# Optimization experiments

Measured on AMD Instinct MI355X. Metric: run time of the kernel, lower is better.

The kernel has to match this reference:

```python
import jax, jax.numpy as jnp
import numpy as np

# Structural hyperparams (mirror init_kwargs)
G, Q, C, D = 2, 8, 1024, 8          # groups, quantizers/group, codebook_size, codebook_dim
DIMS = 1024                          # residual_fsq.dim
DPG = DIMS // G                      # dim per group (project_out output)
B, L = 4, 4096                       # batch, frame length
UP_K, UP_S = 4, 2                    # upsample ConvTranspose1d kernel/stride
HEAD_K, HEAD_OUT = 7, 512            # head Conv1d kernel / out channels


def setup_inputs() -> dict:
    key = jax.random.key(0)
    ks = jax.random.split(key, 8)
    indices = jax.random.randint(ks[0], (B, G * Q, L), 0, C, dtype=jnp.int64)
    codebooks = jax.random.normal(ks[1], (G, Q, C, D), jnp.float32)
    scales = jax.random.uniform(ks[2], (G, Q, D), jnp.float32, 0.5, 2.0)
    W_out = jax.random.normal(ks[3], (G, D, DPG), jnp.float32) * (1.0 / np.sqrt(D))
    b_out = jnp.zeros((G, DPG), jnp.float32)
    W_up = jax.random.normal(ks[4], (DIMS, DIMS, UP_K), jnp.float32) * 0.02   # IOH layout
    b_up = jnp.zeros((DIMS,), jnp.float32)
    W_head = jax.random.normal(ks[5], (HEAD_OUT, DIMS, HEAD_K), jnp.float32) * 0.02  # OIH
    b_head = jnp.zeros((HEAD_OUT,), jnp.float32)
    return dict(indices=indices, codebooks=codebooks, scales=scales,
                W_out=W_out, b_out=b_out, W_up=W_up, b_up=b_up,
                W_head=W_head, b_head=b_head)


def reference(indices, codebooks, scales, W_out, b_out, W_up, b_up, W_head, b_head):
    b, gq, l = indices.shape
    g, q = codebooks.shape[0], codebooks.shape[1]
    # [B, G*Q, L] -> [G, B, L, Q]  (matches view + permute in forward)
    idx = indices.reshape(b, g, q, l).transpose(1, 0, 3, 2)
    mask = idx == -1                              # dropout-padded codes
    idx0 = jnp.where(mask, 0, idx)
    # gather codes per (group, quantizer): codebooks[g, q, idx0[g,b,l,q]] -> [G,B,L,Q,D]
    g_ix = jnp.arange(g)[:, None, None, None]
    q_ix = jnp.arange(q)[None, None, None, :]
    codes = codebooks[g_ix, q_ix, idx0]
    # mask, scale, sum over quantizers (residual sum)
    codes = jnp.where(mask[..., None], 0.0, codes) * scales[:, None, None, :, :]
    summed = codes.sum(axis=3)                    # [G,B,L,D]
    # per-group project_out: Linear(D -> DPG)
    z = jnp.einsum('gbld,gde->gble', summed, W_out) + b_out[:, None, None, :]
    # concat groups along feature dim -> [B, L, DIMS], then NCH for convs
    z_q = z.transpose(1, 2, 0, 3).reshape(b, l, g * z.shape[-1])
    zc = z_q.transpose(0, 2, 1)                   # [B, DIMS, L]
    # upsample: ConvTranspose1d(DIMS->DIMS, k=4, stride=2) -> [B, DIMS, 2L]
    zu = jax.lax.conv_transpose(zc, W_up, strides=(UP_S,), padding='SAME',
                                dimension_numbers=('NCH', 'IOH', 'NCH'))
    zu = zu + b_up[None, :, None]
    # head: Conv1d(DIMS -> HEAD_OUT, k=7, same padding)
    x = jax.lax.conv_general_dilated(zu, W_head, window_strides=(1,), padding='SAME',
                                     dimension_numbers=('NCH', 'OIH', 'NCH'))
    x = x + b_head[None, :, None]
    return x
```

## Files before the change

### kernel.cpp

```cpp
#include <hip/hip_runtime.h>
#include <hip/hip_bf16.h>

typedef __attribute__((ext_vector_type(8))) short bf16x8;
typedef __attribute__((ext_vector_type(4))) float f32x4;

#define GQ 16
#define L_IN 4096
#define T_UP 8192
#define CB 1024
#define ZROWS 4098
#define UROWS 8198

__device__ __forceinline__ void gload16(const void* g, void* l) {
    __builtin_amdgcn_global_load_lds((const __attribute__((address_space(1))) void*)g,
                                     (__attribute__((address_space(3))) void*)l, 16, 0, 0);
}

#define SBR() do { asm volatile("" ::: "memory");                 \
                   __builtin_amdgcn_sched_barrier(0);             \
                   __builtin_amdgcn_s_barrier();                  \
                   __builtin_amdgcn_sched_barrier(0);             \
                   asm volatile("" ::: "memory"); } while (0)
#define LGKM() do { asm volatile("s_waitcnt lgkmcnt(0)" ::: "memory"); \
                    __builtin_amdgcn_sched_barrier(0); } while (0)
#define VMW(n) do { __builtin_amdgcn_sched_barrier(0); \
                    asm volatile("s_waitcnt vmcnt(" #n ")" ::: "memory"); \
                    __builtin_amdgcn_sched_barrier(0); } while (0)

#define MM(MH, NH) do {                                                          \
    __builtin_amdgcn_s_setprio(1);                                               \
    _Pragma("unroll") for (int j_ = 0; j_ < 4; ++j_)                             \
      _Pragma("unroll") for (int n_ = 0; n_ < 2; ++n_)                           \
        _Pragma("unroll") for (int s_ = 0; s_ < 2; ++s_)                         \
          acc[(MH)*4 + j_][(NH)*2 + n_] = __builtin_amdgcn_mfma_f32_16x16x32_bf16( \
              af[j_][s_], bq[(NH)*2 + n_][s_], acc[(MH)*4 + j_][(NH)*2 + n_],    \
              0, 0, 0);                                                          \
    __builtin_amdgcn_s_setprio(0);                                               \
} while (0)

__global__ __launch_bounds__(256) void zero_pads(__hip_bfloat16* __restrict__ zp,
                                                 __hip_bfloat16* __restrict__ zup) {
    int idx = blockIdx.x * 256 + threadIdx.x;
    if (idx < 8192) {
        int b = idx >> 11, rs = (idx >> 10) & 1, c = idx & 1023;
        size_t row = (size_t)b * ZROWS + (rs ? (ZROWS - 1) : 0);
        zp[row * 1024 + c] = __float2bfloat16(0.f);
    } else if (idx < 8192 + 24576) {
        int rem = idx - 8192;
        int b = rem / 6144, r2 = rem % 6144;
        int r6 = r2 >> 10, c = r2 & 1023;
        size_t row = (size_t)b * UROWS + (r6 < 3 ? r6 : (UROWS - 6 + r6));
        zup[row * 1024 + c] = __float2bfloat16(0.f);
    }
}

__global__ __launch_bounds__(256) void repack_up(const float* __restrict__ Wup,
                                                 __hip_bfloat16* __restrict__ Wr) {
    int idx = blockIdx.x * 256 + threadIdx.x;
    int kk = idx >> 20;
    int co = (idx >> 10) & 1023;
    int ci = idx & 1023;
    Wr[idx] = __float2bfloat16(Wup[((ci << 10) + co) * 4 + kk]);
}

__global__ __launch_bounds__(256) void repack_head(const float* __restrict__ Wh,
                                                   __hip_bfloat16* __restrict__ Wr) {
    int idx = blockIdx.x * 256 + threadIdx.x;
    int kk = idx >> 19;
    int rem = idx & ((1 << 19) - 1);
    int o = rem >> 10;
    int ci = rem & 1023;
    Wr[idx] = __float2bfloat16(Wh[(o * 1024 + ci) * 7 + kk]);
}

__global__ __launch_bounds__(256) void dequant_project(
    const int* __restrict__ indices, const float* __restrict__ codebooks,
    const float* __restrict__ scales, const float* __restrict__ Wout,
    const float* __restrict__ bout, __hip_bfloat16* __restrict__ z)
{
    __shared__ float w_lds[8192];
    __shared__ float b_lds[1024];
    __shared__ float part[128];
    __shared__ float summed[16];
    int tid = threadIdx.x;
    for (int k = tid; k < 8192; k += 256) w_lds[k] = Wout[k];
    for (int k = tid; k < 1024; k += 256) b_lds[k] = bout[k];
    int p0 = blockIdx.x * 16;
    int b  = p0 >> 12;
    int l0 = p0 & 4095;
    __syncthreads();
    for (int i = 0; i < 16; ++i) {
        int l = l0 + i;
        if (tid < 128) {
            int gq = tid >> 3;
            int d  = tid & 7;
            int idx = indices[(b * GQ + gq) * L_IN + l];
            float v = 0.f;
            if (idx >= 0) {
                int ic = (idx < CB) ? idx : 0;
                v = codebooks[(gq * CB + ic) * 8 + d] * scales[gq * 8 + d];
            }
            part[tid] = v;
        }
        __syncthreads();
        if (tid < 16) {
            int g = tid >> 3, d = tid & 7;
            float s = 0.f;
            for (int q = 0; q < 8; ++q) s += part[(g * 8 + q) * 8 + d];
            summed[tid] = s;
        }
        __syncthreads();
        #pragma unroll
        for (int j = 0; j < 4; ++j) {
            int c = tid + j * 256;
            int g = c >> 9;
            float acc = b_lds[c];
            #pragma unroll
            for (int d = 0; d < 8; ++d)
                acc += summed[g * 8 + d] * w_lds[(g * 8 + d) * 512 + (c & 511)];
            z[((size_t)b * ZROWS + l + 1) * 1024 + c] = __float2bfloat16(acc);
        }
        __syncthreads();
    }
}


__global__ __launch_bounds__(512, 2) void conv_up_mfma(
    const __hip_bfloat16* __restrict__ zp, const __hip_bfloat16* __restrict__ Wr,
    const float* __restrict__ bup, __hip_bfloat16* __restrict__ zup)
{
    __shared__ __hip_bfloat16 Als[2][256][64];
    __shared__ __hip_bfloat16 Bls[2][256][64];
    const int tid = threadIdx.x;
    const int lane = tid & 63;
    const int w = tid >> 6;
    const int wm = w >> 2, wn = w & 3;
    const int l15 = lane & 15, kq = lane >> 4;
    const int m0  = blockIdx.x * 256;
    const int co0 = blockIdx.y * 256;
    const int b = blockIdx.z >> 1, P = blockIdx.z & 1;
    const int NT = 32, NIT = 16;

    const __hip_bfloat16* abase = zp + ((size_t)b * ZROWS + m0 + P) * 1024;
    const __hip_bfloat16* bbase = Wr + ((size_t)P * 1024 + co0) * 1024;

    auto stage = [&](int kt, int part) {
        if (kt >= NT) return;
        const int buf = kt & 1;
        const int j = kt >> 4, ci0 = (kt & 15) << 6;
        const int rb = (part & 1) << 7;
        const __hip_bfloat16* src;
        __hip_bfloat16* dst;
        if (part < 2) { src = abase + ((size_t)j + rb) * 1024 + ci0;
                        dst = &Als[buf][rb][0]; }
        else          { src = bbase + ((size_t)j * 2048 + rb) * 1024 + ci0;
                        dst = &Bls[buf][rb][0]; }
        #pragma unroll
        for (int it = 0; it < 2; ++it) {
            int chunk = it * 512 + tid;
            int row = chunk >> 3, cs = chunk & 7;
            int cq = cs ^ (row & 7);
            gload16(src + (size_t)row * 1024 + cq * 8,
                    (char*)dst + ((it * 512 + (w << 6)) << 4));
        }
    };

    f32x4 acc[8][4];
    const f32x4 z4 = {0.f, 0.f, 0.f, 0.f};
    #pragma unroll
    for (int i = 0; i < 8; ++i)
        #pragma unroll
        for (int j = 0; j < 4; ++j) acc[i][j] = z4;

    bf16x8 af[4][2], bq[4][2];

    auto rdA = [&](int buf, int mh) {
        #pragma unroll
        for (int j = 0; j < 4; ++j)
            #pragma unroll
            for (int sl = 0; sl < 2; ++sl) {
                int row = (wm << 7) + (mh << 6) + j * 16 + l15;
                int ch = (sl * 4 + kq) ^ (row & 7);
                af[j][sl] = *(const bf16x8*)&Als[buf][row][ch * 8];
            }
    };
    auto rdBlo = [&](int buf) {
        #pragma unroll
        for (int nf = 0; nf < 2; ++nf)
            #pragma unroll
            for (int sl = 0; sl < 2; ++sl) {
                int row = (wn << 6) + nf * 16 + l15;
                int ch = (sl * 4 + kq) ^ (row & 7);
                bq[nf][sl] = *(const bf16x8*)&Bls[buf][row][ch * 8];
            }
    };
    auto rdBhi = [&](int buf) {
        #pragma unroll
        for (int nf = 2; nf < 4; ++nf)
            #pragma unroll
            for (int sl = 0; sl < 2; ++sl) {
                int row = (wn << 6) + nf * 16 + l15;
                int ch = (sl * 4 + kq) ^ (row & 7);
                bq[nf][sl] = *(const bf16x8*)&Bls[buf][row][ch * 8];
            }
    };

    stage(0, 2); stage(0, 3); stage(0, 0); stage(0, 1);
    stage(1, 2); stage(1, 3); stage(1, 0);
    VMW(6);
    SBR();
    rdA(0, 0); rdBlo(0);

    for (int it = 0; it < NIT; ++it) {
        const bool lastit = (it == NIT - 1);
        stage(2 * it + 1, 1);
        SBR(); LGKM();
        MM(0, 0);
        rdBhi(0);
        SBR();
        stage(2 * it + 2, 2);
        SBR(); LGKM();
        MM(0, 1);
        rdA(0, 1);
        SBR();
        stage(2 * it + 2, 3);
        SBR(); LGKM();
        MM(1, 1);
        SBR();
        stage(2 * it + 2, 0);
        if (lastit) { VMW(0); } else { VMW(6); }
        SBR();
        MM(1, 0);
        rdA(1, 0); rdBlo(1);
        SBR();
        stage(2 * it + 2, 1);
        SBR(); LGKM();
        MM(0, 0);
        rdBhi(1);
        SBR();
        stage(2 * it + 3, 2);
        SBR(); LGKM();
        MM(0, 1);
        rdA(1, 1);
        SBR();
        stage(2 * it + 3, 3);
        SBR(); LGKM();
        MM(1, 1);
        SBR();
        stage(2 * it + 3, 0);
        if (!lastit) { VMW(6); }
        SBR();
        MM(1, 0);
        if (!lastit) { rdA(0, 0); rdBlo(0); }
        SBR();
    }

    float bias[4];
    #pragma unroll
    for (int nf = 0; nf < 4; ++nf) bias[nf] = bup[co0 + (wn << 6) + nf * 16 + l15];
    const int mbase = m0 + (wm << 7) + (kq << 2);
    const int cob = co0 + (wn << 6) + l15;
    #pragma unroll
    for (int mf = 0; mf < 8; ++mf)
        #pragma unroll
        for (int e = 0; e < 4; ++e) {
            int m = mbase + mf * 16 + e;
            size_t rowoff = ((size_t)b * UROWS + 3 + P + 2 * m) * 1024;
            #pragma unroll
            for (int nf = 0; nf < 4; ++nf)
                zup[rowoff + cob + nf * 16] = __float2bfloat16(acc[mf][nf][e] + bias[nf]);
        }
}

__global__ __launch_bounds__(512, 2) void conv_head_mfma(
    const __hip_bfloat16* __restrict__ zup, const __hip_bfloat16* __restrict__ Wr,
    const float* __restrict__ bh, float* __restrict__ out)
{
    __shared__ __hip_bfloat16 Als[2][256][64];
    __shared__ __hip_bfloat16 Bls[2][256][64];
    const int tid = threadIdx.x;
    const int lane = tid & 63;
    const int w = tid >> 6;
    const int wm = w >> 2, wn = w & 3;
    const int l15 = lane & 15, kq = lane >> 4;
    const int t0 = blockIdx.x * 256;
    const int o0 = blockIdx.y * 256;
    const int b  = blockIdx.z;
    const int NT = 112, NIT = 56;

    const __hip_bfloat16* bbase = zup + ((size_t)b * UROWS + t0) * 1024;

    auto stage = [&](int kt, int part) {
        if (kt >= NT) return;
        const int buf = kt & 1;
        const int kk = kt >> 4, ci0 = (kt & 15) << 6;
        const int rb = (part & 1) << 7;
        const __hip_bfloat16* src;
        __hip_bfloat16* dst;
        if (part < 2) { src = Wr + ((size_t)(kk * 512 + o0 + rb)) * 1024 + ci0;
                        dst = &Als[buf][rb][0]; }
        else          { src = bbase + ((size_t)(kk + rb)) * 1024 + ci0;
                        dst = &Bls[buf][rb][0]; }
        #pragma unroll
        for (int it = 0; it < 2; ++it) {
            int chunk = it * 512 + tid;
            int row = chunk >> 3, cs = chunk & 7;
            int cq = cs ^ (row & 7);
            gload16(src + (size_t)row * 1024 + cq * 8,
                    (char*)dst + ((it * 512 + (w << 6)) << 4));
        }
    };

    f32x4 acc[8][4];
    const f32x4 z4 = {0.f, 0.f, 0.f, 0.f};
    #pragma unroll
    for (int i = 0; i < 8; ++i)
        #pragma unroll
        for (int j = 0; j < 4; ++j) acc[i][j] = z4;

    bf16x8 af[4][2], bq[4][2];

    auto rdA = [&](int buf, int mh) {
        #pragma unroll
        for (int j = 0; j < 4; ++j)
            #pragma unroll
            for (int sl = 0; sl < 2; ++sl) {
                int row = (wm << 7) + (mh << 6) + j * 16 + l15;
                int ch = (sl * 4 + kq) ^ (row & 7);
                af[j][sl] = *(const bf16x8*)&Als[buf][row][ch * 8];
            }
    };
    auto rdBlo = [&](int buf) {
        #pragma unroll
        for (int nf = 0; nf < 2; ++nf)
            #pragma unroll
            for (int sl = 0; sl < 2; ++sl) {
                int row = (wn << 6) + nf * 16 + l15;
                int ch = (sl * 4 + kq) ^ (row & 7);
                bq[nf][sl] = *(const bf16x8*)&Bls[buf][row][ch * 8];
            }
    };
    auto rdBhi = [&](int buf) {
        #pragma unroll
        for (int nf = 2; nf < 4; ++nf)
            #pragma unroll
            for (int sl = 0; sl < 2; ++sl) {
                int row = (wn << 6) + nf * 16 + l15;
                int ch = (sl * 4 + kq) ^ (row & 7);
                bq[nf][sl] = *(const bf16x8*)&Bls[buf][row][ch * 8];
            }
    };

    stage(0, 2); stage(0, 3); stage(0, 0); stage(0, 1);
    stage(1, 2); stage(1, 3); stage(1, 0);
    VMW(6);
    SBR();
    rdA(0, 0); rdBlo(0);

    for (int it = 0; it < NIT; ++it) {
        const bool lastit = (it == NIT - 1);
        stage(2 * it + 1, 1);
        SBR(); LGKM();
        MM(0, 0);
        rdBhi(0);
        SBR();
        stage(2 * it + 2, 2);
        SBR(); LGKM();
        MM(0, 1);
        rdA(0, 1);
        SBR();
        stage(2 * it + 2, 3);
        SBR(); LGKM();
        MM(1, 1);
        SBR();
        stage(2 * it + 2, 0);
        if (lastit) { VMW(0); } else { VMW(6); }
        SBR();
        MM(1, 0);
        rdA(1, 0); rdBlo(1);
        SBR();
        stage(2 * it + 2, 1);
        SBR(); LGKM();
        MM(0, 0);
        rdBhi(1);
        SBR();
        stage(2 * it + 3, 2);
        SBR(); LGKM();
        MM(0, 1);
        rdA(1, 1);
        SBR();
        stage(2 * it + 3, 3);
        SBR(); LGKM();
        MM(1, 1);
        SBR();
        stage(2 * it + 3, 0);
        if (!lastit) { VMW(6); }
        SBR();
        MM(1, 0);
        if (!lastit) { rdA(0, 0); rdBlo(0); }
        SBR();
    }

    const int obase = o0 + (wm << 7) + (kq << 2);
    const int tbase = t0 + (wn << 6) + l15;
    #pragma unroll
    for (int mf = 0; mf < 8; ++mf)
        #pragma unroll
        for (int e = 0; e < 4; ++e) {
            int o = obase + mf * 16 + e;
            float bias = bh[o];
            size_t rowoff = ((size_t)b * 512 + o) * T_UP + tbase;
            #pragma unroll
            for (int nf = 0; nf < 4; ++nf)
                out[rowoff + nf * 16] = acc[mf][nf][e] + bias;
        }
}

extern "C" void kernel_launch(void* const* d_in, const int* in_sizes, int n_in,
                              void* d_out, int out_size, void* d_ws, size_t ws_size,
                              hipStream_t stream) {
    const int*   indices   = (const int*)d_in[0];
    const float* codebooks = (const float*)d_in[1];
    const float* scales    = (const float*)d_in[2];
    const float* Wout      = (const float*)d_in[3];
    const float* bout      = (const float*)d_in[4];
    const float* Wup       = (const float*)d_in[5];
    const float* bup       = (const float*)d_in[6];
    const float* Wh        = (const float*)d_in[7];
    const float* bh        = (const float*)d_in[8];
    float* out = (float*)d_out;

    __hip_bfloat16* zp    = (__hip_bfloat16*)d_ws;
    __hip_bfloat16* zup   = zp + (size_t)4 * ZROWS * 1024;
    __hip_bfloat16* wr_up = zup + (size_t)4 * UROWS * 1024;
    __hip_bfloat16* wr_h  = wr_up + (size_t)4 * 1024 * 1024;

    zero_pads  <<<dim3(128),   dim3(256), 0, stream>>>(zp, zup);
    repack_up  <<<dim3(16384), dim3(256), 0, stream>>>(Wup, wr_up);
    repack_head<<<dim3(14336), dim3(256), 0, stream>>>(Wh, wr_h);
    dequant_project<<<dim3(1024), dim3(256), 0, stream>>>(indices, codebooks, scales,
                                                          Wout, bout, zp);
    conv_up_mfma  <<<dim3(16, 4, 8), dim3(512), 0, stream>>>(zp, wr_up, bup, zup);
    conv_head_mfma<<<dim3(32, 2, 4), dim3(512), 0, stream>>>(zup, wr_h, bh, out);
}
```

Before: 466.7 us.

## Fold upsample and head convolutions into a single combined-weight GEMM

```diff
diff --git a/kernel.cpp b/kernel.cpp
--- a/kernel.cpp
+++ b/kernel.cpp
@@ -6,10 +6,8 @@
 
 #define GQ 16
 #define L_IN 4096
-#define T_UP 8192
 #define CB 1024
-#define ZROWS 4098
-#define UROWS 8198
+#define ZR 4100
 
 __device__ __forceinline__ void gload16(const void* g, void* l) {
     __builtin_amdgcn_global_load_lds((const __attribute__((address_space(1))) void*)g,
@@ -38,29 +36,17 @@
     __builtin_amdgcn_s_setprio(0);                                               \
 } while (0)
 
-__global__ __launch_bounds__(256) void zero_pads(__hip_bfloat16* __restrict__ zp,
-                                                 __hip_bfloat16* __restrict__ zup) {
+__device__ const int TERM_KK[28]  = {0,1, 0,1,2,3, 2,3,4,5, 4,5,6, 6,
+                                     0, 0,1,2, 1,2,3,4, 3,4,5,6, 5,6};
+__device__ const int TERM_TAP[28] = {1,0, 3,2,1,0, 3,2,1,0, 3,2,1, 3,
+                                     0, 2,1,0, 3,2,1,0, 3,2,1,0, 3,2};
+__device__ const int SLICE_OFF[11] = {0,2,6,10,13,14,15,18,22,26,28};
+
+__global__ __launch_bounds__(256) void zero_pads_z(__hip_bfloat16* __restrict__ zp) {
     int idx = blockIdx.x * 256 + threadIdx.x;
-    if (idx < 8192) {
-        int b = idx >> 11, rs = (idx >> 10) & 1, c = idx & 1023;
-        size_t row = (size_t)b * ZROWS + (rs ? (ZROWS - 1) : 0);
-        zp[row * 1024 + c] = __float2bfloat16(0.f);
-    } else if (idx < 8192 + 24576) {
-        int rem = idx - 8192;
-        int b = rem / 6144, r2 = rem % 6144;
-        int r6 = r2 >> 10, c = r2 & 1023;
-        size_t row = (size_t)b * UROWS + (r6 < 3 ? r6 : (UROWS - 6 + r6));
-        zup[row * 1024 + c] = __float2bfloat16(0.f);
-    }
-}
-
-__global__ __launch_bounds__(256) void repack_up(const float* __restrict__ Wup,
-                                                 __hip_bfloat16* __restrict__ Wr) {
-    int idx = blockIdx.x * 256 + threadIdx.x;
-    int kk = idx >> 20;
-    int co = (idx >> 10) & 1023;
-    int ci = idx & 1023;
-    Wr[idx] = __float2bfloat16(Wup[((ci << 10) + co) * 4 + kk]);
+    int b = idx >> 12, r4 = (idx >> 10) & 3, c = idx & 1023;
+    size_t row = (size_t)b * ZR + (r4 < 2 ? r4 : (ZR - 4 + r4));
+    zp[row * 1024 + c] = __float2bfloat16(0.f);
 }
 
 __global__ __launch_bounds__(256) void repack_head(const float* __restrict__ Wh,
@@ -69,8 +55,18 @@
     int kk = idx >> 19;
     int rem = idx & ((1 << 19) - 1);
     int o = rem >> 10;
-    int ci = rem & 1023;
-    Wr[idx] = __float2bfloat16(Wh[(o * 1024 + ci) * 7 + kk]);
+    int cu = rem & 1023;
+    Wr[idx] = __float2bfloat16(Wh[(o * 1024 + cu) * 7 + kk]);
+}
+
+__global__ __launch_bounds__(256) void repack_upT(const float* __restrict__ Wup,
+                                                  __hip_bfloat16* __restrict__ Wupt) {
+    int idx = blockIdx.x * 256 + threadIdx.x;
+    const float4 w = *(const float4*)&Wup[(size_t)idx * 4];
+    Wupt[idx]           = __float2bfloat16(w.x);
+    Wupt[1048576 + idx] = __float2bfloat16(w.y);
+    Wupt[2097152 + idx] = __float2bfloat16(w.z);
+    Wupt[3145728 + idx] = __float2bfloat16(w.w);
 }
 
 __global__ __launch_bounds__(256) void dequant_project(
@@ -118,16 +114,31 @@
             #pragma unroll
             for (int d = 0; d < 8; ++d)
                 acc += summed[g * 8 + d] * w_lds[(g * 8 + d) * 512 + (c & 511)];
-            z[((size_t)b * ZROWS + l + 1) * 1024 + c] = __float2bfloat16(acc);
+            z[((size_t)b * ZR + l + 2) * 1024 + c] = __float2bfloat16(acc);
         }
         __syncthreads();
     }
 }
 
-
-__global__ __launch_bounds__(512, 2) void conv_up_mfma(
-    const __hip_bfloat16* __restrict__ zp, const __hip_bfloat16* __restrict__ Wr,
-    const float* __restrict__ bup, __hip_bfloat16* __restrict__ zup)
+__global__ __launch_bounds__(64) void bias_combine(const float* __restrict__ Wh,
+                                                   const float* __restrict__ bup,
+                                                   const float* __restrict__ bh,
+                                                   float* __restrict__ bt) {
+    int o = blockIdx.x * 64 + threadIdx.x;
+    float acc = bh[o];
+    const float* wrow = Wh + (size_t)o * 7168;
+    for (int cu = 0; cu < 1024; ++cu) {
+        float ws = 0.f;
+        #pragma unroll
+        for (int kk = 0; kk < 7; ++kk) ws += wrow[cu * 7 + kk];
+        acc += ws * bup[cu];
+    }
+    bt[o] = acc;
+}
+
+__global__ __launch_bounds__(512, 2) void combine_gemm(
+    const __hip_bfloat16* __restrict__ Whr, const __hip_bfloat16* __restrict__ Wupt,
+    float* __restrict__ P32)
 {
     __shared__ __hip_bfloat16 Als[2][256][64];
     __shared__ __hip_bfloat16 Bls[2][256][64];
@@ -136,25 +147,24 @@
     const int w = tid >> 6;
     const int wm = w >> 2, wn = w & 3;
     const int l15 = lane & 15, kq = lane >> 4;
-    const int m0  = blockIdx.x * 256;
-    const int co0 = blockIdx.y * 256;
-    const int b = blockIdx.z >> 1, P = blockIdx.z & 1;
-    const int NT = 32, NIT = 16;
-
-    const __hip_bfloat16* abase = zp + ((size_t)b * ZROWS + m0 + P) * 1024;
-    const __hip_bfloat16* bbase = Wr + ((size_t)P * 1024 + co0) * 1024;
+    const int g   = blockIdx.x;
+    const int o0  = blockIdx.y * 256;
+    const int cz0 = blockIdx.z * 256;
+    const int NT = 16, NIT = 8;
+    const int kk = TERM_KK[g], tap = TERM_TAP[g];
+
+    const __hip_bfloat16* abase = Whr + ((size_t)kk * 512 + o0) * 1024;
+    const __hip_bfloat16* bbase = Wupt + ((size_t)tap * 1024 + cz0) * 1024;
 
     auto stage = [&](int kt, int part) {
         if (kt >= NT) return;
         const int buf = kt & 1;
-        const int j = kt >> 4, ci0 = (kt & 15) << 6;
+        const int ci0 = (kt & 15) << 6;
         const int rb = (part & 1) << 7;
         const __hip_bfloat16* src;
         __hip_bfloat16* dst;
-        if (part < 2) { src = abase + ((size_t)j + rb) * 1024 + ci0;
-                        dst = &Als[buf][rb][0]; }
-        else          { src = bbase + ((size_t)j * 2048 + rb) * 1024 + ci0;
-                        dst = &Bls[buf][rb][0]; }
+        if (part < 2) { src = abase + (size_t)rb * 1024 + ci0; dst = &Als[buf][rb][0]; }
+        else          { src = bbase + (size_t)rb * 1024 + ci0; dst = &Bls[buf][rb][0]; }
         #pragma unroll
         for (int it = 0; it < 2; ++it) {
             int chunk = it * 512 + tid;
@@ -255,26 +265,34 @@
         SBR();
     }
 
-    float bias[4];
-    #pragma unroll
-    for (int nf = 0; nf < 4; ++nf) bias[nf] = bup[co0 + (wn << 6) + nf * 16 + l15];
-    const int mbase = m0 + (wm << 7) + (kq << 2);
-    const int cob = co0 + (wn << 6) + l15;
+    const int obase = o0 + (wm << 7) + (kq << 2);
+    const int czb = cz0 + (wn << 6) + l15;
+    float* pg = P32 + (size_t)g * (512 * 1024);
     #pragma unroll
     for (int mf = 0; mf < 8; ++mf)
         #pragma unroll
         for (int e = 0; e < 4; ++e) {
-            int m = mbase + mf * 16 + e;
-            size_t rowoff = ((size_t)b * UROWS + 3 + P + 2 * m) * 1024;
+            size_t rowoff = (size_t)(obase + mf * 16 + e) * 1024;
             #pragma unroll
             for (int nf = 0; nf < 4; ++nf)
-                zup[rowoff + cob + nf * 16] = __float2bfloat16(acc[mf][nf][e] + bias[nf]);
-        }
-}
-
-__global__ __launch_bounds__(512, 2) void conv_head_mfma(
-    const __hip_bfloat16* __restrict__ zup, const __hip_bfloat16* __restrict__ Wr,
-    const float* __restrict__ bh, float* __restrict__ out)
+                pg[rowoff + czb + nf * 16] = acc[mf][nf][e];
+        }
+}
+
+__global__ __launch_bounds__(256) void reduce_cc(const float* __restrict__ P32,
+                                                 __hip_bfloat16* __restrict__ CC) {
+    int idx = blockIdx.x * 256 + threadIdx.x;
+    int s = idx >> 19;
+    int r = idx & 524287;
+    float sum = 0.f;
+    for (int g = SLICE_OFF[s]; g < SLICE_OFF[s + 1]; ++g)
+        sum += P32[(size_t)g * 524288 + r];
+    CC[idx] = __float2bfloat16(sum);
+}
+
+__global__ __launch_bounds__(512, 2) void fused_main(
+    const __hip_bfloat16* __restrict__ zp, const __hip_bfloat16* __restrict__ CC,
+    const float* __restrict__ bt, float* __restrict__ out)
 {
     __shared__ __hip_bfloat16 Als[2][256][64];
     __shared__ __hip_bfloat16 Bls[2][256][64];
@@ -283,23 +301,24 @@
     const int w = tid >> 6;
     const int wm = w >> 2, wn = w & 3;
     const int l15 = lane & 15, kq = lane >> 4;
-    const int t0 = blockIdx.x * 256;
+    const int m0 = blockIdx.x * 256;
     const int o0 = blockIdx.y * 256;
-    const int b  = blockIdx.z;
-    const int NT = 112, NIT = 56;
-
-    const __hip_bfloat16* bbase = zup + ((size_t)b * UROWS + t0) * 1024;
+    const int b = blockIdx.z >> 1, P = blockIdx.z & 1;
+    const int NT = 80, NIT = 40;
+
+    const __hip_bfloat16* abase = CC + (size_t)P * 5 * 512 * 1024;
+    const __hip_bfloat16* bbase = zp + ((size_t)b * ZR + m0) * 1024;
 
     auto stage = [&](int kt, int part) {
         if (kt >= NT) return;
         const int buf = kt & 1;
-        const int kk = kt >> 4, ci0 = (kt & 15) << 6;
+        const int j = kt >> 4, ci0 = (kt & 15) << 6;
         const int rb = (part & 1) << 7;
         const __hip_bfloat16* src;
         __hip_bfloat16* dst;
-        if (part < 2) { src = Wr + ((size_t)(kk * 512 + o0 + rb)) * 1024 + ci0;
+        if (part < 2) { src = abase + ((size_t)(j * 512 + o0 + rb)) * 1024 + ci0;
                         dst = &Als[buf][rb][0]; }
-        else          { src = bbase + ((size_t)(kk + rb)) * 1024 + ci0;
+        else          { src = bbase + ((size_t)(j + rb)) * 1024 + ci0;
                         dst = &Bls[buf][rb][0]; }
         #pragma unroll
         for (int it = 0; it < 2; ++it) {
@@ -402,18 +421,60 @@
     }
 
     const int obase = o0 + (wm << 7) + (kq << 2);
-    const int tbase = t0 + (wn << 6) + l15;
+    const int tb = m0 + (wn << 6) + l15;
     #pragma unroll
     for (int mf = 0; mf < 8; ++mf)
         #pragma unroll
         for (int e = 0; e < 4; ++e) {
             int o = obase + mf * 16 + e;
-            float bias = bh[o];
-            size_t rowoff = ((size_t)b * 512 + o) * T_UP + tbase;
+            float bias = bt[o];
+            size_t rowoff = ((size_t)(b * 512 + o)) * 8192 + P;
             #pragma unroll
             for (int nf = 0; nf < 4; ++nf)
-                out[rowoff + nf * 16] = acc[mf][nf][e] + bias;
-        }
+                out[rowoff + 2 * (tb + nf * 16)] = acc[mf][nf][e] + bias;
+        }
+}
+
+__global__ __launch_bounds__(512) void fixup(const __hip_bfloat16* __restrict__ zp,
+                                             const __hip_bfloat16* __restrict__ Wupt,
+                                             const __hip_bfloat16* __restrict__ Whr,
+                                             float* __restrict__ out) {
+    __shared__ float zl[1024];
+    __shared__ float vsh[1024];
+    const int tid = threadIdx.x;
+    const int side = blockIdx.x & 1, b = blockIdx.x >> 1;
+    const int zrow = side ? 4097 : 2;
+    const int tap  = side ? 0 : 3;
+    zl[tid]       = __bfloat162float(zp[((size_t)b * ZR + zrow) * 1024 + tid]);
+    zl[tid + 512] = __bfloat162float(zp[((size_t)b * ZR + zrow) * 1024 + tid + 512]);
+    __syncthreads();
+    float a0 = 0.f, a1 = 0.f;
+    const __hip_bfloat16* wt = Wupt + (size_t)tap * 1048576;
+    for (int cz = 0; cz < 1024; ++cz) {
+        float zv = zl[cz];
+        a0 += zv * __bfloat162float(wt[(size_t)cz * 1024 + tid]);
+        a1 += zv * __bfloat162float(wt[(size_t)cz * 1024 + tid + 512]);
+    }
+    vsh[tid] = a0; vsh[tid + 512] = a1;
+    __syncthreads();
+    const int lane = tid & 63, wv = tid >> 6;
+    float vr[16];
+    #pragma unroll
+    for (int e = 0; e < 16; ++e) vr[e] = vsh[lane * 16 + e];
+    for (int tt = 0; tt < 3; ++tt) {
+        int t  = side ? (8189 + tt) : tt;
+        int kk = side ? (6 - tt) : (2 - tt);
+        for (int oo = 0; oo < 64; ++oo) {
+            int o = wv * 64 + oo;
+            const __hip_bfloat16* wr = Whr + ((size_t)kk * 512 + o) * 1024 + lane * 16;
+            float p = 0.f;
+            #pragma unroll
+            for (int e = 0; e < 16; ++e) p += __bfloat162float(wr[e]) * vr[e];
+            #pragma unroll
+            for (int s = 32; s > 0; s >>= 1) p += __shfl_xor(p, s, 64);
+            if (lane == 0) out[((size_t)(b * 512 + o)) * 8192 + t] -= p;
+        }
+    }
 }
 
 extern "C" void kernel_launch(void* const* d_in, const int* in_sizes, int n_in,
@@ -430,16 +491,21 @@
     const float* bh        = (const float*)d_in[8];
     float* out = (float*)d_out;
 
-    __hip_bfloat16* zp    = (__hip_bfloat16*)d_ws;
-    __hip_bfloat16* zup   = zp + (size_t)4 * ZROWS * 1024;
-    __hip_bfloat16* wr_up = zup + (size_t)4 * UROWS * 1024;
-    __hip_bfloat16* wr_h  = wr_up + (size_t)4 * 1024 * 1024;
-
-    zero_pads  <<<dim3(128),   dim3(256), 0, stream>>>(zp, zup);
-    repack_up  <<<dim3(16384), dim3(256), 0, stream>>>(Wup, wr_up);
-    repack_head<<<dim3(14336), dim3(256), 0, stream>>>(Wh, wr_h);
+    __hip_bfloat16* zp   = (__hip_bfloat16*)d_ws;
+    __hip_bfloat16* whr  = zp + (size_t)4 * ZR * 1024;
+    __hip_bfloat16* wupt = whr + (size_t)7 * 512 * 1024;
+    __hip_bfloat16* cc   = wupt + (size_t)4 * 1024 * 1024;
+    float* p32 = (float*)(cc + (size_t)10 * 512 * 1024);
+    float* bt  = p32 + (size_t)28 * 512 * 1024;
+
+    zero_pads_z   <<<dim3(64),    dim3(256), 0, stream>>>(zp);
+    repack_head   <<<dim3(14336), dim3(256), 0, stream>>>(Wh, whr);
+    repack_upT    <<<dim3(4096),  dim3(256), 0, stream>>>(Wup, wupt);
     dequant_project<<<dim3(1024), dim3(256), 0, stream>>>(indices, codebooks, scales,
                                                           Wout, bout, zp);
-    conv_up_mfma  <<<dim3(16, 4, 8), dim3(512), 0, stream>>>(zp, wr_up, bup, zup);
-    conv_head_mfma<<<dim3(32, 2, 4), dim3(512), 0, stream>>>(zup, wr_h, bh, out);
-}
+    bias_combine  <<<dim3(8),     dim3(64),  0, stream>>>(Wh, bup, bh, bt);
+    combine_gemm  <<<dim3(28, 2, 4), dim3(512), 0, stream>>>(whr, wupt, p32);
+    reduce_cc     <<<dim3(20480), dim3(256), 0, stream>>>(p32, cc);
+    fused_main    <<<dim3(16, 2, 8), dim3(512), 0, stream>>>(zp, cc, bt, out);
+    fixup         <<<dim3(8),     dim3(512), 0, stream>>>(zp, wupt, whr, out);
+}
```

Result: slower. 647.7 us (+38.8%).
